# Kernel tuning notes

Measured on AMD Instinct MI355X. Metric: run time of the kernel, lower is better.

The kernel has to match this reference:

```python
import jax, jax.numpy as jnp
import numpy as np

N_EMBD = 1024
HEAD_SIZE = 64

def setup_inputs() -> dict:
    key = jax.random.key(0)
    kx, kk, kq, kv = jax.random.split(key, 4)
    x = jax.random.normal(kx, (8, 2048, N_EMBD), dtype=jnp.float32)
    scale = 1.0 / np.sqrt(N_EMBD)
    # nn.Linear weights are [out, in]; kaiming-uniform-ish init
    Wk = jax.random.uniform(kk, (HEAD_SIZE, N_EMBD), dtype=jnp.float32, minval=-scale, maxval=scale)
    Wq = jax.random.uniform(kq, (HEAD_SIZE, N_EMBD), dtype=jnp.float32, minval=-scale, maxval=scale)
    Wv = jax.random.uniform(kv, (HEAD_SIZE, N_EMBD), dtype=jnp.float32, minval=-scale, maxval=scale)
    return {"x": x, "Wk": Wk, "Wq": Wq, "Wv": Wv}

def reference(x, Wk, Wq, Wv):
    # x: [B, T, E]; W*: [H, E] (torch Linear layout)
    k = jnp.einsum('bte,he->bth', x, Wk)
    q = jnp.einsum('bte,he->bth', x, Wq)
    v = jnp.einsum('bte,he->bth', x, Wv)
    inv_sqrt_h = 1.0 / np.sqrt(HEAD_SIZE)
    wei = jnp.einsum('bth,bsh->bts', q, k) * inv_sqrt_h  # [B, T, T]
    wei = jax.nn.softmax(wei, axis=-1)
    out = jnp.einsum('bts,bsh->bth', wei, v)  # [B, T, H]
    return out
```

## Files before the change

kernel.cpp:

```cpp
#include <hip/hip_runtime.h>
#include <cstdint>

#define NB 8
#define TS 2048
#define NE 1024
#define HD 64
#define MTOT (NB*TS)

typedef float     f4  __attribute__((ext_vector_type(4)));
typedef short     s8v __attribute__((ext_vector_type(8)));
typedef short     s4v __attribute__((ext_vector_type(4)));
typedef int       i4v __attribute__((ext_vector_type(4)));
typedef _Float16  h8  __attribute__((ext_vector_type(8)));

__device__ __forceinline__ short f2bf(float f) {
  union { float f; uint32_t u; } x; x.f = f;
  return (short)((x.u + 0x7FFFu + ((x.u >> 16) & 1u)) >> 16);
}

__device__ __forceinline__ int pack2(float lo, float hi) {
  union { float f; uint32_t u; } a, b; a.f = lo; b.f = hi;
  return (int)__builtin_amdgcn_perm(b.u + 0x8000u, a.u + 0x8000u, 0x07060302u);
}

__device__ __forceinline__ void gl2lds(const void* gptr, void* lptr) {
  auto g = (const __attribute__((address_space(1))) uint32_t*)gptr;
  auto l = (__attribute__((address_space(3))) uint32_t*)lptr;
  __builtin_amdgcn_global_load_lds(g, l, 16, 0, 0);
}

template <int N>
__device__ __forceinline__ void wait_barrier() {
  asm volatile("s_waitcnt vmcnt(%0) lgkmcnt(0)" :: "n"(N) : "memory");
  __builtin_amdgcn_s_barrier();
}

__global__ __launch_bounds__(256) void wconv_kernel(
    const float* __restrict__ Wk, const float* __restrict__ Wq, const float* __restrict__ Wv,
    short* __restrict__ wb)
{
  const int idx = (blockIdx.x * 256 + threadIdx.x) * 4;
  const int p = idx >> 16;
  const int off = idx & 65535;
  const float* W = (p == 0) ? Wq : (p == 1) ? Wk : Wv;
  const float s = (p == 0) ? 0.18033688011112042f : 1.0f;
  const float4 v = *(const float4*)&W[off];
  s4v h; h[0] = f2bf(v.x*s); h[1] = f2bf(v.y*s); h[2] = f2bf(v.z*s); h[3] = f2bf(v.w*s);
  *(s4v*)&wb[idx] = h;
}

__global__ __launch_bounds__(256) void proj_kernel(
    const float* __restrict__ x, const short* __restrict__ wb,
    short* __restrict__ qo, short* __restrict__ ko, _Float16* __restrict__ vo)
{
  __shared__ float Xs[4][32][64];
  __shared__ short Ws[2][192][64];
  const int tid = threadIdx.x;
  const int wv = tid >> 6, lane = tid & 63, n = lane & 15, quad = lane >> 4;
  const int mg = wv & 1, cg = wv >> 1;
  const int r0 = blockIdx.x * 32;
  const int xrow = lane >> 4, xslot = lane & 15;
  const int wrow = lane >> 3, wslot = lane & 7;

  auto dmaX = [&](int c, int buf) {
#pragma unroll
    for (int u = 0; u < 2; ++u) {
      const int R0 = (wv * 2 + u) * 4;
      const int row = R0 + xrow;
      const int gs = (xslot + row) & 15;
      gl2lds(&x[(size_t)(r0 + row) * NE + c * 64 + gs * 4], &Xs[buf][R0][0]);
    }
  };
  auto dmaW = [&](int c, int buf) {
#pragma unroll
    for (int u = 0; u < 6; ++u) {
      const int C0 = (wv * 6 + u) * 8;
      const int col = C0 + wrow;
      const int gs = (wslot + col) & 7;
      gl2lds(&wb[(size_t)col * NE + c * 64 + gs * 8], &Ws[buf][C0][0]);
    }
  };

  const f4 fz = {0.f, 0.f, 0.f, 0.f};
  f4 acc[6] = {fz, fz, fz, fz, fz, fz};

  auto compute = [&](int bw, int bx) {
    s8v a[2];
    const int row = mg * 16 + n;
#pragma unroll
    for (int kc = 0; kc < 2; ++kc) {
      const int u0 = kc * 8 + quad * 2;
      const float* pr = &Xs[bx][row][0];
      const f4 f0 = *(const f4*)(pr + (((u0    ) - row) & 15) * 4);
      const f4 f1 = *(const f4*)(pr + (((u0 + 1) - row) & 15) * 4);
      i4v ai;
      ai[0] = pack2(f0[0], f0[1]); ai[1] = pack2(f0[2], f0[3]);
      ai[2] = pack2(f1[0], f1[1]); ai[3] = pack2(f1[2], f1[3]);
      a[kc] = __builtin_bit_cast(s8v, ai);
    }
#pragma unroll
    for (int nf = 0; nf < 6; ++nf) {
      const int col = cg * 96 + nf * 16 + n;
      const s8v b0 = *(const s8v*)&Ws[bw][col][(((0 + quad) - col) & 7) * 8];
      const s8v b1 = *(const s8v*)&Ws[bw][col][(((4 + quad) - col) & 7) * 8];
      acc[nf] = __builtin_amdgcn_mfma_f32_16x16x32_bf16(a[0], b0, acc[nf], 0, 0, 0);
      acc[nf] = __builtin_amdgcn_mfma_f32_16x16x32_bf16(a[1], b1, acc[nf], 0, 0, 0);
    }
  };

  dmaW(0, 0); dmaX(0, 0); dmaX(1, 1); dmaX(2, 2);
  wait_barrier<4>();

  for (int t = 0; t < 16; ++t) {
    if (t <= 14) dmaW(t + 1, (t + 1) & 1);
    if (t <= 12) dmaX(t + 3, (t + 3) & 3);
    compute(t & 1, t & 3);
    if (t <= 12)      wait_barrier<2>();
    else if (t <= 14) wait_barrier<0>();
  }

#pragma unroll
  for (int nf = 0; nf < 6; ++nf) {
    const int gc = cg * 96 + nf * 16;
    const int p = gc >> 6;
    const int rcol = (gc & 63) + n;
#pragma unroll
    for (int i = 0; i < 4; ++i) {
      const int R = r0 + mg * 16 + quad * 4 + i;
      const float av = acc[nf][i];
      if (p == 0)      qo[(size_t)R * HD + rcol] = f2bf(av);
      else if (p == 1) ko[(size_t)R * HD + rcol] = f2bf(av);
      else {
        const int t2 = R & (TS - 1), b = t2 & 31;
        const int pos = (t2 & ~31) | (((b >> 2) & 3) << 3) | (((b >> 4) & 1) << 2) | (b & 3);
        vo[(size_t)(R >> 11) * HD * TS + (size_t)rcol * TS + pos] = (_Float16)av;
      }
    }
  }
}

__global__ __launch_bounds__(256) void attn_kernel(
    const short* __restrict__ q, const short* __restrict__ k,
    const _Float16* __restrict__ vT, float* __restrict__ out)
{
  __shared__ __align__(16) char smem[65536];
  const int tid = threadIdx.x;
  const int wv = tid >> 6, lane = tid & 63, n = lane & 15, quad = lane >> 4;
  const int half = wv >> 1, qw = wv & 1;
  const int batch = blockIdx.x & 7;
  const int qg = blockIdx.x >> 3;
  const int m0 = batch * TS + qg * 32;
  const short*    kb = k  + (size_t)batch * TS * HD;
  const _Float16* vb = vT + (size_t)batch * HD * TS;
  const f4 fz = {0.f, 0.f, 0.f, 0.f};

  auto kbuf = [&](int b) { return (short*)   (smem +         (half * 2 + b) * 8192); };
  auto vbuf = [&](int b) { return (_Float16*)(smem + 32768 + (half * 2 + b) * 8192); };

  auto dmaKV = [&](int t) {
    const int b = t & 1;
    const int c0 = half * 1024 + t * 64;
    short*    kd = kbuf(b);
    _Float16* vd = vbuf(b);
#pragma unroll
    for (int u = 0; u < 4; ++u) {
      const int K0 = qw * 32 + u * 8;
      const int key = K0 + (lane >> 3);
      const int s = lane & 7;
      gl2lds(&kb[(size_t)(c0 + key) * HD + (((s + key) & 7) << 3)], kd + K0 * 64);
    }
#pragma unroll
    for (int u = 0; u < 4; ++u) {
      const int D0 = qw * 32 + u * 8;
      const int d = D0 + (lane >> 3);
      const int s = lane & 7;
      gl2lds(&vb[(size_t)d * TS + c0 + (((s + d) & 7) << 3)], vd + D0 * 64);
    }
  };

  s8v qf[2];
#pragma unroll
  for (int kc = 0; kc < 2; ++kc)
    qf[kc] = *(const s8v*)&q[(size_t)(m0 + qw * 16 + n) * HD + kc * 32 + quad * 8];

  f4 o[4] = {fz, fz, fz, fz};
  f4 lD = fz;
  h8 ones;
#pragma unroll
  for (int j = 0; j < 8; ++j) ones[j] = (_Float16)1.0f;

  dmaKV(0);
  wait_barrier<0>();

  for (int t = 0; t < 16; ++t) {
    const int buf = t & 1;
    if (t < 15) dmaKV(t + 1);

    const short*    ks = kbuf(buf);
    const _Float16* vs = vbuf(buf);

    s8v kf[4][2];
#pragma unroll
    for (int f = 0; f < 4; ++f)
#pragma unroll
      for (int kc = 0; kc < 2; ++kc) {
        const int key = f * 16 + n;
        kf[f][kc] = *(const s8v*)&ks[key * 64 + (((kc * 4 + quad) - key) & 7) * 8];
      }

    f4 st[4];
#pragma unroll
    for (int f = 0; f < 4; ++f) {
      st[f] = __builtin_amdgcn_mfma_f32_16x16x32_bf16(kf[f][0], qf[0], fz, 0, 0, 0);
      st[f] = __builtin_amdgcn_mfma_f32_16x16x32_bf16(kf[f][1], qf[1], st[f], 0, 0, 0);
    }

    h8 pa[2];
#pragma unroll
    for (int pr = 0; pr < 2; ++pr)
#pragma unroll
      for (int hf = 0; hf < 2; ++hf)
#pragma unroll
        for (int i = 0; i < 4; ++i)
          pa[pr][hf * 4 + i] = (_Float16)__builtin_amdgcn_exp2f(st[pr * 2 + hf][i]);

#pragma unroll
    for (int pr = 0; pr < 2; ++pr) {
      lD = __builtin_amdgcn_mfma_f32_16x16x32_f16(pa[pr], ones, lD, 0, 0, 0);
#pragma unroll
      for (int g = 0; g < 4; ++g) {
        const int d = g * 16 + n;
        const h8 vf = *(const h8*)&vs[d * 64 + (((pr * 4 + quad) - d) & 7) * 8];
        o[g] = __builtin_amdgcn_mfma_f32_16x16x32_f16(pa[pr], vf, o[g], 0, 0, 0);
      }
    }

    if (t < 15) wait_barrier<0>();
  }

  __syncthreads();

  float* o_c = (float*)smem;
  float* l_c = (float*)(smem + 17408);
  if (n == 0)
#pragma unroll
    for (int i = 0; i < 4; ++i) l_c[wv * 16 + quad * 4 + i] = lD[i];
#pragma unroll
  for (int g = 0; g < 4; ++g)
#pragma unroll
    for (int i = 0; i < 4; ++i)
      o_c[(wv * 16 + quad * 4 + i) * 68 + g * 16 + n] = o[g][i];
  __syncthreads();

  const int qr = tid >> 3, d8 = (tid & 7) * 8;
  const int qw2 = qr >> 4, wr = qr & 15;
  const float L = l_c[qw2 * 16 + wr] + l_c[(2 + qw2) * 16 + wr];
  const float inv = 1.0f / L;
  f4 s0 = *(const f4*)&o_c[(qw2 * 16 + wr) * 68 + d8];
  f4 s1 = *(const f4*)&o_c[(qw2 * 16 + wr) * 68 + d8 + 4];
  s0 += *(const f4*)&o_c[((2 + qw2) * 16 + wr) * 68 + d8];
  s1 += *(const f4*)&o_c[((2 + qw2) * 16 + wr) * 68 + d8 + 4];
  s0 *= inv; s1 *= inv;
  *(f4*)&out[(size_t)(m0 + qr) * HD + d8]     = s0;
  *(f4*)&out[(size_t)(m0 + qr) * HD + d8 + 4] = s1;
}

extern "C" void kernel_launch(void* const* d_in, const int* in_sizes, int n_in,
                              void* d_out, int out_size, void* d_ws, size_t ws_size,
                              hipStream_t stream) {
  const float* x  = (const float*)d_in[0];
  const float* Wk = (const float*)d_in[1];
  const float* Wq = (const float*)d_in[2];
  const float* Wv = (const float*)d_in[3];
  float* out = (float*)d_out;

  short* qb = (short*)d_ws;
  short* kb = qb + (size_t)MTOT * HD;
  _Float16* vb = (_Float16*)(kb + (size_t)MTOT * HD);
  short* wb = (short*)(vb + (size_t)NB * HD * TS);

  wconv_kernel<<<192, 256, 0, stream>>>(Wk, Wq, Wv, wb);
  proj_kernel<<<MTOT / 32, 256, 0, stream>>>(x, wb, qb, kb, vb);
  attn_kernel<<<MTOT / 32, 256, 0, stream>>>(qb, kb, vb, out);
}
```

Measured before the change: 131.5 us.

## Deepen async copy pipelines with smaller K-chunks in projection and attention

Both the projection and attention kernels switch from 64-wide chunks with double or quad buffering to 32-wide chunks with deeper ring buffers. Prefetch now runs two chunks ahead for W and K/V, and four ahead for X, with partial wait counts in place of full drains. The aim is to hide global-to-LDS latency and stop each iteration stalling on a full wait. In exchange the loops run twice as many iterations with more barriers, the LDS swizzles change, and projection LDS use grows to 80KB, which may lower occupancy.

```diff
diff --git a/kernel.cpp b/kernel.cpp
--- a/kernel.cpp
+++ b/kernel.cpp
@@ -53,70 +53,66 @@
     const float* __restrict__ x, const short* __restrict__ wb,
     short* __restrict__ qo, short* __restrict__ ko, _Float16* __restrict__ vo)
 {
-  __shared__ float Xs[4][32][64];
-  __shared__ short Ws[2][192][64];
+  __shared__ __align__(16) char smem[81920];
+  float (*Xs)[32][32] = (float (*)[32][32])smem;
+  short (*Ws)[192][32] = (short (*)[192][32])(smem + 32768);
+
   const int tid = threadIdx.x;
   const int wv = tid >> 6, lane = tid & 63, n = lane & 15, quad = lane >> 4;
   const int mg = wv & 1, cg = wv >> 1;
   const int r0 = blockIdx.x * 32;
-  const int xrow = lane >> 4, xslot = lane & 15;
-  const int wrow = lane >> 3, wslot = lane & 7;
-
-  auto dmaX = [&](int c, int buf) {
-#pragma unroll
-    for (int u = 0; u < 2; ++u) {
-      const int R0 = (wv * 2 + u) * 4;
-      const int row = R0 + xrow;
-      const int gs = (xslot + row) & 15;
-      gl2lds(&x[(size_t)(r0 + row) * NE + c * 64 + gs * 4], &Xs[buf][R0][0]);
-    }
-  };
-  auto dmaW = [&](int c, int buf) {
-#pragma unroll
-    for (int u = 0; u < 6; ++u) {
-      const int C0 = (wv * 6 + u) * 8;
-      const int col = C0 + wrow;
-      const int gs = (wslot + col) & 7;
-      gl2lds(&wb[(size_t)col * NE + c * 64 + gs * 8], &Ws[buf][C0][0]);
+
+  auto dmaX = [&](int c) {
+    const int row = wv * 8 + (lane >> 3);
+    const int s = lane & 7;
+    const int gs = (s + row) & 7;
+    gl2lds(&x[(size_t)(r0 + row) * NE + c * 32 + gs * 4], &Xs[c & 7][wv * 8][0]);
+  };
+  auto dmaW = [&](int c) {
+#pragma unroll
+    for (int u = 0; u < 3; ++u) {
+      const int C0 = wv * 48 + u * 16;
+      const int col = C0 + (lane >> 2);
+      const int s = lane & 3;
+      const int gs = (s + col + (col >> 2)) & 3;
+      gl2lds(&wb[(size_t)col * NE + c * 32 + gs * 8], &Ws[c & 3][C0][0]);
     }
   };
 
   const f4 fz = {0.f, 0.f, 0.f, 0.f};
   f4 acc[6] = {fz, fz, fz, fz, fz, fz};
 
-  auto compute = [&](int bw, int bx) {
-    s8v a[2];
+  auto compute = [&](int t) {
+    const int bx = t & 7, bw = t & 3;
     const int row = mg * 16 + n;
-#pragma unroll
-    for (int kc = 0; kc < 2; ++kc) {
-      const int u0 = kc * 8 + quad * 2;
-      const float* pr = &Xs[bx][row][0];
-      const f4 f0 = *(const f4*)(pr + (((u0    ) - row) & 15) * 4);
-      const f4 f1 = *(const f4*)(pr + (((u0 + 1) - row) & 15) * 4);
-      i4v ai;
-      ai[0] = pack2(f0[0], f0[1]); ai[1] = pack2(f0[2], f0[3]);
-      ai[2] = pack2(f1[0], f1[1]); ai[3] = pack2(f1[2], f1[3]);
-      a[kc] = __builtin_bit_cast(s8v, ai);
-    }
+    const float* pr = &Xs[bx][row][0];
+    const int u0 = quad * 2;
+    const f4 f0 = *(const f4*)(pr + (((u0    ) - row) & 7) * 4);
+    const f4 f1 = *(const f4*)(pr + (((u0 + 1) - row) & 7) * 4);
+    i4v ai;
+    ai[0] = pack2(f0[0], f0[1]); ai[1] = pack2(f0[2], f0[3]);
+    ai[2] = pack2(f1[0], f1[1]); ai[3] = pack2(f1[2], f1[3]);
+    const s8v af = __builtin_bit_cast(s8v, ai);
 #pragma unroll
     for (int nf = 0; nf < 6; ++nf) {
       const int col = cg * 96 + nf * 16 + n;
-      const s8v b0 = *(const s8v*)&Ws[bw][col][(((0 + quad) - col) & 7) * 8];
-      const s8v b1 = *(const s8v*)&Ws[bw][col][(((4 + quad) - col) & 7) * 8];
-      acc[nf] = __builtin_amdgcn_mfma_f32_16x16x32_bf16(a[0], b0, acc[nf], 0, 0, 0);
-      acc[nf] = __builtin_amdgcn_mfma_f32_16x16x32_bf16(a[1], b1, acc[nf], 0, 0, 0);
-    }
-  };
-
-  dmaW(0, 0); dmaX(0, 0); dmaX(1, 1); dmaX(2, 2);
-  wait_barrier<4>();
-
-  for (int t = 0; t < 16; ++t) {
-    if (t <= 14) dmaW(t + 1, (t + 1) & 1);
-    if (t <= 12) dmaX(t + 3, (t + 3) & 3);
-    compute(t & 1, t & 3);
-    if (t <= 12)      wait_barrier<2>();
-    else if (t <= 14) wait_barrier<0>();
+      const s8v bf = *(const s8v*)&Ws[bw][col][((quad - col - (col >> 2)) & 3) * 8];
+      acc[nf] = __builtin_amdgcn_mfma_f32_16x16x32_bf16(af, bf, acc[nf], 0, 0, 0);
+    }
+  };
+
+  dmaW(0); dmaX(0); dmaW(1); dmaX(1); dmaX(2); dmaX(3);
+  wait_barrier<6>();
+
+  for (int t = 0; t < 32; ++t) {
+    if (t < 30) dmaW(t + 2);
+    if (t < 28) dmaX(t + 4);
+    compute(t);
+    if (t == 0)       wait_barrier<6>();
+    else if (t <= 27) wait_barrier<5>();
+    else if (t == 28) wait_barrier<4>();
+    else if (t == 29) wait_barrier<3>();
+    else if (t == 30) wait_barrier<0>();
   }
 
 #pragma unroll
@@ -154,27 +150,26 @@
   const _Float16* vb = vT + (size_t)batch * HD * TS;
   const f4 fz = {0.f, 0.f, 0.f, 0.f};
 
-  auto kbuf = [&](int b) { return (short*)   (smem +         (half * 2 + b) * 8192); };
-  auto vbuf = [&](int b) { return (_Float16*)(smem + 32768 + (half * 2 + b) * 8192); };
+  auto kbuf = [&](int b) { return (short*)   (smem +         (half * 4 + b) * 4096); };
+  auto vbuf = [&](int b) { return (_Float16*)(smem + 32768 + (half * 4 + b) * 4096); };
 
   auto dmaKV = [&](int t) {
-    const int b = t & 1;
-    const int c0 = half * 1024 + t * 64;
-    short*    kd = kbuf(b);
-    _Float16* vd = vbuf(b);
-#pragma unroll
-    for (int u = 0; u < 4; ++u) {
-      const int K0 = qw * 32 + u * 8;
+    const int b = t & 3;
+    const int c0 = half * 1024 + t * 32;
+#pragma unroll
+    for (int u = 0; u < 2; ++u) {
+      const int K0 = qw * 16 + u * 8;
       const int key = K0 + (lane >> 3);
       const int s = lane & 7;
-      gl2lds(&kb[(size_t)(c0 + key) * HD + (((s + key) & 7) << 3)], kd + K0 * 64);
-    }
-#pragma unroll
-    for (int u = 0; u < 4; ++u) {
-      const int D0 = qw * 32 + u * 8;
-      const int d = D0 + (lane >> 3);
-      const int s = lane & 7;
-      gl2lds(&vb[(size_t)d * TS + c0 + (((s + d) & 7) << 3)], vd + D0 * 64);
+      gl2lds(&kb[(size_t)(c0 + key) * HD + (((s + key) & 7) << 3)], kbuf(b) + K0 * 64);
+    }
+#pragma unroll
+    for (int u = 0; u < 2; ++u) {
+      const int D0 = qw * 32 + u * 16;
+      const int d = D0 + (lane >> 2);
+      const int s = lane & 3;
+      const int gs = (s + d + (d >> 2)) & 3;
+      gl2lds(&vb[(size_t)d * TS + c0 + gs * 8], vbuf(b) + D0 * 32);
     }
   };
 
@@ -189,53 +184,48 @@
 #pragma unroll
   for (int j = 0; j < 8; ++j) ones[j] = (_Float16)1.0f;
 
-  dmaKV(0);
-  wait_barrier<0>();
-
-  for (int t = 0; t < 16; ++t) {
-    const int buf = t & 1;
-    if (t < 15) dmaKV(t + 1);
-
-    const short*    ks = kbuf(buf);
-    const _Float16* vs = vbuf(buf);
-
-    s8v kf[4][2];
-#pragma unroll
-    for (int f = 0; f < 4; ++f)
-#pragma unroll
-      for (int kc = 0; kc < 2; ++kc) {
-        const int key = f * 16 + n;
-        kf[f][kc] = *(const s8v*)&ks[key * 64 + (((kc * 4 + quad) - key) & 7) * 8];
+  dmaKV(0); dmaKV(1);
+  wait_barrier<4>();
+
+  for (int t = 0; t < 32; ++t) {
+    if (t < 30) dmaKV(t + 2);
+    {
+      const short*    ks = kbuf(t & 3);
+      const _Float16* vs = vbuf(t & 3);
+
+      s8v kf[2][2];
+#pragma unroll
+      for (int f = 0; f < 2; ++f)
+#pragma unroll
+        for (int kc = 0; kc < 2; ++kc) {
+          const int key = f * 16 + n;
+          kf[f][kc] = *(const s8v*)&ks[key * 64 + (((kc * 4 + quad) - key) & 7) * 8];
+        }
+
+      f4 st[2];
+#pragma unroll
+      for (int f = 0; f < 2; ++f) {
+        st[f] = __builtin_amdgcn_mfma_f32_16x16x32_bf16(kf[f][0], qf[0], fz, 0, 0, 0);
+        st[f] = __builtin_amdgcn_mfma_f32_16x16x32_bf16(kf[f][1], qf[1], st[f], 0, 0, 0);
       }
 
-    f4 st[4];
-#pragma unroll
-    for (int f = 0; f < 4; ++f) {
-      st[f] = __builtin_amdgcn_mfma_f32_16x16x32_bf16(kf[f][0], qf[0], fz, 0, 0, 0);
-      st[f] = __builtin_amdgcn_mfma_f32_16x16x32_bf16(kf[f][1], qf[1], st[f], 0, 0, 0);
-    }
-
-    h8 pa[2];
-#pragma unroll
-    for (int pr = 0; pr < 2; ++pr)
+      h8 pa;
 #pragma unroll
       for (int hf = 0; hf < 2; ++hf)
 #pragma unroll
         for (int i = 0; i < 4; ++i)
-          pa[pr][hf * 4 + i] = (_Float16)__builtin_amdgcn_exp2f(st[pr * 2 + hf][i]);
-
-#pragma unroll
-    for (int pr = 0; pr < 2; ++pr) {
-      lD = __builtin_amdgcn_mfma_f32_16x16x32_f16(pa[pr], ones, lD, 0, 0, 0);
+          pa[hf * 4 + i] = (_Float16)__builtin_amdgcn_exp2f(st[hf][i]);
+
+      lD = __builtin_amdgcn_mfma_f32_16x16x32_f16(pa, ones, lD, 0, 0, 0);
 #pragma unroll
       for (int g = 0; g < 4; ++g) {
         const int d = g * 16 + n;
-        const h8 vf = *(const h8*)&vs[d * 64 + (((pr * 4 + quad) - d) & 7) * 8];
-        o[g] = __builtin_amdgcn_mfma_f32_16x16x32_f16(pa[pr], vf, o[g], 0, 0, 0);
+        const h8 vf = *(const h8*)&vs[d * 32 + ((quad - d - (d >> 2)) & 3) * 8];
+        o[g] = __builtin_amdgcn_mfma_f32_16x16x32_f16(pa, vf, o[g], 0, 0, 0);
       }
     }
-
-    if (t < 15) wait_barrier<0>();
+    if (t < 30)       wait_barrier<4>();
+    else if (t == 30) wait_barrier<0>();
   }
 
   __syncthreads();
```

New measurement: 139.4 us. 1.06x slower.
